# Performance work log

Hardware: AMD Instinct MI355X
Metric: run time of the kernel (lower is better)

The kernel has to match this reference:

```python
import jax, jax.numpy as jnp
import numpy as np

N_NODES = 50000
N_EDGES = 800000
N_GRAPHS = 512
IN_FEATS = 256
HIDDEN = 128
OUT_FEATS = 128


def _lin(key, fan_in, fan_out):
    return jax.random.normal(key, (fan_in, fan_out), jnp.float32) * (1.0 / np.sqrt(fan_in))


def setup_inputs() -> dict:
    key = jax.random.key(0)
    ks = jax.random.split(key, 16)
    x = jax.random.normal(ks[0], (N_NODES, IN_FEATS), jnp.float32)
    edge_index = jax.random.randint(ks[1], (2, N_EDGES), 0, N_NODES, jnp.int32)
    batch = jnp.sort(jax.random.randint(ks[2], (N_NODES,), 0, N_GRAPHS, jnp.int32))
    return {
        "x": x,
        "edge_index": edge_index,
        "batch": batch,
        "num_graphs": N_GRAPHS,
        # TD branch GCN params
        "td_W1": _lin(ks[3], IN_FEATS, HIDDEN), "td_b1": jnp.zeros((HIDDEN,), jnp.float32),
        "td_W2": _lin(ks[4], HIDDEN, OUT_FEATS), "td_b2": jnp.zeros((OUT_FEATS,), jnp.float32),
        # BU branch GCN params
        "bu_W1": _lin(ks[5], IN_FEATS, HIDDEN), "bu_b1": jnp.zeros((HIDDEN,), jnp.float32),
        "bu_W2": _lin(ks[6], HIDDEN, OUT_FEATS), "bu_b2": jnp.zeros((OUT_FEATS,), jnp.float32),
        # proj_head: Linear(256,256) -> ReLU -> Linear(256,128)
        "pw1": _lin(ks[7], OUT_FEATS * 2, 256), "pb1": jnp.zeros((256,), jnp.float32),
        "pw2": _lin(ks[8], 256, 128), "pb2": jnp.zeros((128,), jnp.float32),
    }


def gcn_conv(h_in, W, b, src, dst, n_nodes):
    """PyG GCNConv: self-loops + symmetric normalization D^-1/2 (A+I) D^-1/2 X W + b."""
    h = h_in @ W  # [N, out]
    ones = jnp.ones(src.shape[0], h.dtype)
    deg = jax.ops.segment_sum(ones, dst, num_segments=n_nodes) + 1.0  # +1 for self-loop
    dinv = jax.lax.rsqrt(deg)  # deg >= 1 always
    norm = dinv[src] * dinv[dst]  # [E]
    agg = jax.ops.segment_sum(h[src] * norm[:, None], dst, num_segments=n_nodes)
    agg = agg + h * (dinv * dinv)[:, None]  # self-loop edge contribution
    return agg + b


def reference(x, edge_index, batch, num_graphs,
              td_W1, td_b1, td_W2, td_b2,
              bu_W1, bu_b1, bu_W2, bu_b2,
              pw1, pb1, pw2, pb2):
    n = x.shape[0]
    src, dst = edge_index[0], edge_index[1]

    def branch(W1, b1, W2, b2, s, d):
        h = jax.nn.relu(gcn_conv(x, W1, b1, s, d, n))
        # dropout is identity in eval mode
        h = gcn_conv(h, W2, b2, s, d, n)
        return jax.ops.segment_sum(h, batch, num_segments=num_graphs)  # global_add_pool

    td = branch(td_W1, td_b1, td_W2, td_b2, src, dst)
    bu = branch(bu_W1, bu_b1, bu_W2, bu_b2, dst, src)  # flipped edge_index
    h = jnp.concatenate([bu, td], axis=1)  # [G, 2*out_feats]
    h = jax.nn.relu(h @ pw1 + pb1) @ pw2 + pb2
    return h
```

## Files before the change

kernel.cpp:

```cpp
#include <hip/hip_runtime.h>

#define N_NODES 50000
#define N_PAD   50048
#define N_EDGES 800000
#define N_GRAPHS 512
#define F_IN 256
#define F_H 128
#define F_CAT 256

#define BSHIFT 9
#define NB 98
#define CAP 10240
#define EPB 3125

typedef __attribute__((ext_vector_type(8))) short short8;
typedef __attribute__((ext_vector_type(4))) float f32x4;
typedef unsigned int uint;
typedef unsigned short ushort;

static __device__ __forceinline__ ushort f2bf(float f) {
    uint u = __float_as_uint(f);
    u += 0x7FFF + ((u >> 16) & 1);
    return (ushort)(u >> 16);
}
static __device__ __forceinline__ float bflo(uint v) { return __uint_as_float(v << 16); }
static __device__ __forceinline__ float bfhi(uint v) { return __uint_as_float(v & 0xFFFF0000u); }
static __device__ __forceinline__ float bfu(ushort v) { return __uint_as_float((uint)v << 16); }

#define GLL(g, l) __builtin_amdgcn_global_load_lds( \
    (const __attribute__((address_space(1))) unsigned int*)(g), \
    (__attribute__((address_space(3))) unsigned int*)(l), 16, 0, 0)

__global__ __launch_bounds__(256) void csr_scatter_kernel(
        const int* __restrict__ ei, int* __restrict__ gcur,
        uint* __restrict__ ebuf_td, uint* __restrict__ ebuf_bu) {
    __shared__ int lcnt[256];
    __shared__ int lbase[256];
    int tid = threadIdx.x;
    lcnt[tid] = 0;
    __syncthreads();
    int e0 = blockIdx.x * EPB;
    for (int k = tid; k < EPB; k += 256) {
        int i = e0 + k;
        int s = ei[i], d = ei[N_EDGES + i];
        atomicAdd(&lcnt[d >> BSHIFT], 1);
        atomicAdd(&lcnt[128 + (s >> BSHIFT)], 1);
    }
    __syncthreads();
    if (tid < 2 * NB) {
        int dir = tid / NB, b = tid % NB;
        int c = lcnt[dir * 128 + b];
        lbase[dir * 128 + b] = c ? atomicAdd(&gcur[dir * NB + b], c) : 0;
    }
    __syncthreads();
    lcnt[tid] = 0;
    __syncthreads();
    for (int k = tid; k < EPB; k += 256) {
        int i = e0 + k;
        int s = ei[i], d = ei[N_EDGES + i];
        int bd = d >> BSHIFT, bs = s >> BSHIFT;
        int p = atomicAdd(&lcnt[bd], 1) + lbase[bd];
        ebuf_td[(size_t)bd * CAP + p] = (uint)s | ((uint)(d & 511) << 16);
        int q = atomicAdd(&lcnt[128 + bs], 1) + lbase[128 + bs];
        ebuf_bu[(size_t)bs * CAP + q] = (uint)d | ((uint)(s & 511) << 16);
    }
}

__global__ __launch_bounds__(256) void csr_build_kernel(
        const uint* __restrict__ ebuf_td, const uint* __restrict__ ebuf_bu,
        const int* __restrict__ gcur,
        int* off_td, int* off_bu, ushort* deg_td, ushort* deg_bu,
        float* dinv_td, float* dinv_bu, ushort* csr_td, ushort* csr_bu) {
    int b = blockIdx.x, dir = blockIdx.y;
    const uint* ebuf = dir ? ebuf_bu : ebuf_td;
    int* off     = dir ? off_bu : off_td;
    ushort* deg  = dir ? deg_bu : deg_td;
    float* dinv  = dir ? dinv_bu : dinv_td;
    ushort* csr  = dir ? csr_bu : csr_td;
    __shared__ int cntL[512], offL[512], sm[256];
    int tid = threadIdx.x;
    cntL[tid] = 0; cntL[tid + 256] = 0;
    __syncthreads();
    int rbeg = b * CAP;
    int rend = rbeg + gcur[dir * NB + b];
    for (int k = rbeg + tid; k < rend; k += 256)
        atomicAdd(&cntL[ebuf[k] >> 16], 1);
    __syncthreads();
    int a0 = cntL[tid * 2], a1 = cntL[tid * 2 + 1];
    int ps = a0 + a1;
    sm[tid] = ps;
    __syncthreads();
    for (int o = 1; o < 256; o <<= 1) {
        int u = (tid >= o) ? sm[tid - o] : 0;
        __syncthreads();
        sm[tid] += u;
        __syncthreads();
    }
    int excl = sm[tid] - ps;
    offL[tid * 2] = excl;
    offL[tid * 2 + 1] = excl + a0;
    __syncthreads();
    int nbase = b << BSHIFT;
#pragma unroll
    for (int j = 0; j < 2; j++) {
        int nloc = tid + j * 256;
        int n = nbase + nloc;
        if (n < N_NODES) {
            off[n] = rbeg + offL[nloc];
            int c = cntL[nloc];
            deg[n] = (ushort)c;
            dinv[n] = rsqrtf((float)c + 1.0f);
        }
    }
    cntL[tid] = offL[tid];
    cntL[tid + 256] = offL[tid + 256];
    __syncthreads();
    for (int k = rbeg + tid; k < rend; k += 256) {
        uint e = ebuf[k];
        int slot = atomicAdd(&cntL[e >> 16], 1);
        csr[rbeg + slot] = (ushort)(e & 0xFFFF);
    }
}

__global__ void cvt_x_kernel(const float* __restrict__ x, ushort* __restrict__ xb) {
    size_t i = (size_t)blockIdx.x * blockDim.x + threadIdx.x;
    ushort4 u = {0, 0, 0, 0};
    if (i < (size_t)N_NODES * (F_IN / 4)) {
        float4 f = ((const float4*)x)[i];
        u.x = f2bf(f.x); u.y = f2bf(f.y); u.z = f2bf(f.z); u.w = f2bf(f.w);
    }
    ((ushort4*)xb)[i] = u;
}

__global__ void prep_w_kernel(const float* __restrict__ td_W1, const float* __restrict__ bu_W1,
                              const float* __restrict__ td_W2, const float* __restrict__ bu_W2,
                              ushort* __restrict__ Bt1, ushort* __restrict__ Wt2) {
    int n = blockIdx.x;
    int k = threadIdx.x;
    float w1 = (n < F_H) ? td_W1[(size_t)k * F_H + n] : bu_W1[(size_t)k * F_H + (n - F_H)];
    Bt1[(size_t)n * 256 + k] = f2bf(w1);
    if (k < 128) {
        float w2 = (n < F_H) ? bu_W2[(size_t)k * F_H + n]
                             : td_W2[(size_t)k * F_H + (n - F_H)];
        Wt2[(size_t)k * 256 + n] = f2bf(w2);
    }
}

__global__ __launch_bounds__(256) void gemm_mfma(
        const ushort* __restrict__ A, const ushort* __restrict__ Bt,
        ushort* __restrict__ C,
        const float* __restrict__ dinv_td, const float* __restrict__ dinv_bu) {
    __shared__ __align__(16) ushort As[128 * 32];
    __shared__ __align__(16) ushort Bs[128 * 32];
    int tid = threadIdx.x;
    int wave = tid >> 6, lane = tid & 63, quad = lane >> 4, l16 = lane & 15;
    size_t bm = (size_t)blockIdx.x * 128;
    size_t bn = (size_t)blockIdx.y * 128;
    const float* dsel = blockIdx.y ? dinv_bu : dinv_td;

    f32x4 acc[2][8];
    const f32x4 z4 = {0.f, 0.f, 0.f, 0.f};
#pragma unroll
    for (int i = 0; i < 2; i++)
#pragma unroll
        for (int j = 0; j < 8; j++) acc[i][j] = z4;

    int cb0 = wave * 64;
    int cb1 = 256 + wave * 64;
    int c0 = cb0 + lane, c1 = cb1 + lane;
    int r0 = c0 >> 2, s0 = (c0 & 3) * 8;
    int r1 = c1 >> 2, s1 = (c1 & 3) * 8;
    const ushort* a0p = A + (bm + r0) * 256 + s0;
    const ushort* a1p = A + (bm + r1) * 256 + s1;
    const ushort* b0p = Bt + (bn + r0) * 256 + s0;
    const ushort* b1p = Bt + (bn + r1) * 256 + s1;
    ushort* lA0 = As + cb0 * 8;
    ushort* lA1 = As + cb1 * 8;
    ushort* lB0 = Bs + cb0 * 8;
    ushort* lB1 = Bs + cb1 * 8;

    for (int kb = 0; kb < 8; kb++) {
        int k0 = kb * 32;
        __syncthreads();
        GLL(a0p + k0, lA0);
        GLL(a1p + k0, lA1);
        GLL(b0p + k0, lB0);
        GLL(b1p + k0, lB1);
        __syncthreads();
        short8 af0 = *(const short8*)(As + (wave * 32 + l16) * 32 + quad * 8);
        short8 af1 = *(const short8*)(As + (wave * 32 + 16 + l16) * 32 + quad * 8);
#pragma unroll
        for (int ct = 0; ct < 8; ct++) {
            short8 bfr = *(const short8*)(Bs + (ct * 16 + l16) * 32 + quad * 8);
            acc[0][ct] = __builtin_amdgcn_mfma_f32_16x16x32_bf16(af0, bfr, acc[0][ct], 0, 0, 0);
            acc[1][ct] = __builtin_amdgcn_mfma_f32_16x16x32_bf16(af1, bfr, acc[1][ct], 0, 0, 0);
        }
    }
#pragma unroll
    for (int rt = 0; rt < 2; rt++) {
#pragma unroll
        for (int r = 0; r < 4; r++) {
            size_t row = bm + wave * 32 + rt * 16 + quad * 4 + r;
            float dv = dsel[row];
#pragma unroll
            for (int ct = 0; ct < 8; ct++) {
                C[row * 256 + bn + ct * 16 + l16] = f2bf(acc[rt][ct][r] * dv);
            }
        }
    }
}

static __device__ __forceinline__ void gather_node(
        const ushort* __restrict__ base, const ushort* __restrict__ csr,
        int kb, int ke, int half, float a[4]) {
    float p[4] = {0.f, 0.f, 0.f, 0.f};
    float q[4] = {0.f, 0.f, 0.f, 0.f};
    float r[4] = {0.f, 0.f, 0.f, 0.f};
    int k = kb;
    for (; k + 16 <= ke; k += 16) {
        int i0 = csr[k + half],      i1 = csr[k + 2 + half];
        int i2 = csr[k + 4 + half],  i3 = csr[k + 6 + half];
        int i4 = csr[k + 8 + half],  i5 = csr[k + 10 + half];
        int i6 = csr[k + 12 + half], i7 = csr[k + 14 + half];
        uint2 v0 = *(const uint2*)(base + (size_t)i0 * F_CAT);
        uint2 v1 = *(const uint2*)(base + (size_t)i1 * F_CAT);
        uint2 v2 = *(const uint2*)(base + (size_t)i2 * F_CAT);
        uint2 v3 = *(const uint2*)(base + (size_t)i3 * F_CAT);
        uint2 v4 = *(const uint2*)(base + (size_t)i4 * F_CAT);
        uint2 v5 = *(const uint2*)(base + (size_t)i5 * F_CAT);
        uint2 v6 = *(const uint2*)(base + (size_t)i6 * F_CAT);
        uint2 v7 = *(const uint2*)(base + (size_t)i7 * F_CAT);
        a[0] += bflo(v0.x); a[1] += bfhi(v0.x); a[2] += bflo(v0.y); a[3] += bfhi(v0.y);
        p[0] += bflo(v1.x); p[1] += bfhi(v1.x); p[2] += bflo(v1.y); p[3] += bfhi(v1.y);
        q[0] += bflo(v2.x); q[1] += bfhi(v2.x); q[2] += bflo(v2.y); q[3] += bfhi(v2.y);
        r[0] += bflo(v3.x); r[1] += bfhi(v3.x); r[2] += bflo(v3.y); r[3] += bfhi(v3.y);
        a[0] += bflo(v4.x); a[1] += bfhi(v4.x); a[2] += bflo(v4.y); a[3] += bfhi(v4.y);
        p[0] += bflo(v5.x); p[1] += bfhi(v5.x); p[2] += bflo(v5.y); p[3] += bfhi(v5.y);
        q[0] += bflo(v6.x); q[1] += bfhi(v6.x); q[2] += bflo(v6.y); q[3] += bfhi(v6.y);
        r[0] += bflo(v7.x); r[1] += bfhi(v7.x); r[2] += bflo(v7.y); r[3] += bfhi(v7.y);
    }
    for (; k + 8 <= ke; k += 8) {
        int i0 = csr[k + half],     i1 = csr[k + 2 + half];
        int i2 = csr[k + 4 + half], i3 = csr[k + 6 + half];
        uint2 v0 = *(const uint2*)(base + (size_t)i0 * F_CAT);
        uint2 v1 = *(const uint2*)(base + (size_t)i1 * F_CAT);
        uint2 v2 = *(const uint2*)(base + (size_t)i2 * F_CAT);
        uint2 v3 = *(const uint2*)(base + (size_t)i3 * F_CAT);
        a[0] += bflo(v0.x); a[1] += bfhi(v0.x); a[2] += bflo(v0.y); a[3] += bfhi(v0.y);
        p[0] += bflo(v1.x); p[1] += bfhi(v1.x); p[2] += bflo(v1.y); p[3] += bfhi(v1.y);
        q[0] += bflo(v2.x); q[1] += bfhi(v2.x); q[2] += bflo(v2.y); q[3] += bfhi(v2.y);
        r[0] += bflo(v3.x); r[1] += bfhi(v3.x); r[2] += bflo(v3.y); r[3] += bfhi(v3.y);
    }
    for (; k < ke; k += 2) {
        int kk = k + half;
        if (kk < ke) {
            uint2 v = *(const uint2*)(base + (size_t)csr[kk] * F_CAT);
            a[0] += bflo(v.x); a[1] += bfhi(v.x); a[2] += bflo(v.y); a[3] += bfhi(v.y);
        }
    }
#pragma unroll
    for (int j = 0; j < 4; j++) a[j] += (p[j] + q[j]) + r[j];
}

__global__ __launch_bounds__(256) void agg1_kernel(
        const ushort* __restrict__ linS, ushort* __restrict__ h1s,
        const ushort* __restrict__ csr_td, const int* __restrict__ off_td,
        const ushort* __restrict__ deg_td, const float* __restrict__ dinv_td,
        const ushort* __restrict__ csr_bu, const int* __restrict__ off_bu,
        const ushort* __restrict__ deg_bu, const float* __restrict__ dinv_bu,
        const float* __restrict__ b_td, const float* __restrict__ b_bu) {
    int wave = threadIdx.x >> 6, lane = threadIdx.x & 63;
    int n0 = (blockIdx.x * 2 + (wave >> 1)) * 8;
    int br = wave & 1;
    const ushort* csr = br ? csr_bu : csr_td;
    const int* off    = br ? off_bu : off_td;
    const ushort* deg = br ? deg_bu : deg_td;
    const float* dinv = br ? dinv_bu : dinv_td;
    const float* bias = br ? b_bu : b_td;
    int half = lane >> 5, l32 = lane & 31;
    int col = br * F_H + l32 * 4;
    const ushort* base = linS + col;
    int bcol = l32 * 4;
    float bs0 = bias[bcol], bs1 = bias[bcol + 1];
    float bs2 = bias[bcol + 2], bs3 = bias[bcol + 3];

#pragma unroll
    for (int j = 0; j < 8; j++) {
        int n = n0 + j;
        float a[4] = {0.f, 0.f, 0.f, 0.f};
        int kb = off[n];
        gather_node(base, csr, kb, kb + deg[n], half, a);
#pragma unroll
        for (int t = 0; t < 4; t++) a[t] += __shfl_xor(a[t], 32);
        uint2 vs = *(const uint2*)(base + (size_t)n * F_CAT);
        a[0] += bflo(vs.x); a[1] += bfhi(vs.x); a[2] += bflo(vs.y); a[3] += bfhi(vs.y);
        float dn = dinv[n];
        float o0 = fmaxf(a[0] * dn + bs0, 0.f) * dn;
        float o1 = fmaxf(a[1] * dn + bs1, 0.f) * dn;
        float o2 = fmaxf(a[2] * dn + bs2, 0.f) * dn;
        float o3 = fmaxf(a[3] * dn + bs3, 0.f) * dn;
        if (half == 0) {
            uint2 pk;
            pk.x = (uint)f2bf(o0) | ((uint)f2bf(o1) << 16);
            pk.y = (uint)f2bf(o2) | ((uint)f2bf(o3) << 16);
            *(uint2*)(h1s + (size_t)n * F_CAT + col) = pk;
        }
    }
}

__global__ __launch_bounds__(256) void agg2_pool_kernel(
        const ushort* __restrict__ h1s, float* __restrict__ pooled_pre,
        const int* __restrict__ batch,
        const ushort* __restrict__ csr_td, const int* __restrict__ off_td,
        const ushort* __restrict__ deg_td, const float* __restrict__ dinv_td,
        const ushort* __restrict__ csr_bu, const int* __restrict__ off_bu,
        const ushort* __restrict__ deg_bu, const float* __restrict__ dinv_bu) {
    int wave = threadIdx.x >> 6, lane = threadIdx.x & 63;
    int n0 = (blockIdx.x * 2 + (wave >> 1)) * 8;
    int br = wave & 1;
    const ushort* csr = br ? csr_bu : csr_td;
    const int* off    = br ? off_bu : off_td;
    const ushort* deg = br ? deg_bu : deg_td;
    const float* dinv = br ? dinv_bu : dinv_td;
    int half = lane >> 5, l32 = lane & 31;
    int col = br * F_H + l32 * 4;
    const ushort* base = h1s + col;

    float acc0 = 0.f, acc1 = 0.f, acc2 = 0.f, acc3 = 0.f;
    int gcur = batch[n0];
#pragma unroll
    for (int j = 0; j < 8; j++) {
        int n = n0 + j;
        int g = batch[n];
        if (g != gcur) {
            if (half == 0) {
                float* pp = &pooled_pre[(size_t)gcur * F_CAT + col];
                unsafeAtomicAdd(pp,     acc0);
                unsafeAtomicAdd(pp + 1, acc1);
                unsafeAtomicAdd(pp + 2, acc2);
                unsafeAtomicAdd(pp + 3, acc3);
            }
            acc0 = acc1 = acc2 = acc3 = 0.f;
            gcur = g;
        }
        float a[4] = {0.f, 0.f, 0.f, 0.f};
        int kb = off[n];
        gather_node(base, csr, kb, kb + deg[n], half, a);
#pragma unroll
        for (int t = 0; t < 4; t++) a[t] += __shfl_xor(a[t], 32);
        uint2 vs = *(const uint2*)(base + (size_t)n * F_CAT);
        a[0] += bflo(vs.x); a[1] += bfhi(vs.x); a[2] += bflo(vs.y); a[3] += bfhi(vs.y);
        float dn = dinv[n];
        acc0 += a[0] * dn;
        acc1 += a[1] * dn;
        acc2 += a[2] * dn;
        acc3 += a[3] * dn;
    }
    if (half == 0) {
        float* pp = &pooled_pre[(size_t)gcur * F_CAT + col];
        unsafeAtomicAdd(pp,     acc0);
        unsafeAtomicAdd(pp + 1, acc1);
        unsafeAtomicAdd(pp + 2, acc2);
        unsafeAtomicAdd(pp + 3, acc3);
    }
}

__global__ __launch_bounds__(256) void head_kernel(
        const float* __restrict__ pooled_pre, const int* __restrict__ batch,
        const ushort* __restrict__ Wt2,
        const float* __restrict__ td_b2, const float* __restrict__ bu_b2,
        const float* __restrict__ pw1, const float* __restrict__ pb1,
        const float* __restrict__ pw2, const float* __restrict__ pb2,
        float* __restrict__ out) {
    int g = blockIdx.x;
    int tid = threadIdx.x;
    __shared__ float row[256], z[256], hid[256];
    row[tid] = pooled_pre[(size_t)g * 256 + tid];
    int lo = 0, hi = N_NODES;
    while (lo < hi) { int m = (lo + hi) >> 1; if (batch[m] < g) lo = m + 1; else hi = m; }
    int start = lo;
    lo = start; hi = N_NODES;
    while (lo < hi) { int m = (lo + hi) >> 1; if (batch[m] < g + 1) lo = m + 1; else hi = m; }
    float cnt = (float)(lo - start);
    __syncthreads();
    const float* rsel = (tid < 128) ? (row + F_H) : row;
    float b2 = (tid < 128) ? bu_b2[tid] : td_b2[tid - F_H];
    float acc = cnt * b2;
    for (int k = 0; k < F_H; k++) acc += rsel[k] * bfu(Wt2[(size_t)k * 256 + tid]);
    z[tid] = acc;
    __syncthreads();
    float h = pb1[tid];
    for (int k = 0; k < 256; k++) h += z[k] * pw1[(size_t)k * 256 + tid];
    hid[tid] = fmaxf(h, 0.f);
    __syncthreads();
    if (tid < 128) {
        float o = pb2[tid];
        for (int k = 0; k < 256; k++) o += hid[k] * pw2[(size_t)k * 128 + tid];
        out[(size_t)g * 128 + tid] = o;
    }
}

extern "C" void kernel_launch(void* const* d_in, const int* in_sizes, int n_in,
                              void* d_out, int out_size, void* d_ws, size_t ws_size,
                              hipStream_t stream) {
    const float* x     = (const float*)d_in[0];
    const int*   ei    = (const int*)d_in[1];
    const int*   batch = (const int*)d_in[2];
    const float* td_W1 = (const float*)d_in[4];
    const float* td_b1 = (const float*)d_in[5];
    const float* td_W2 = (const float*)d_in[6];
    const float* td_b2 = (const float*)d_in[7];
    const float* bu_W1 = (const float*)d_in[8];
    const float* bu_b1 = (const float*)d_in[9];
    const float* bu_W2 = (const float*)d_in[10];
    const float* bu_b2 = (const float*)d_in[11];
    const float* pw1   = (const float*)d_in[12];
    const float* pb1   = (const float*)d_in[13];
    const float* pw2   = (const float*)d_in[14];
    const float* pb2   = (const float*)d_in[15];
    float* out = (float*)d_out;

    char* p = (char*)d_ws;
    auto alloc = [&](size_t bytes) { void* r = (void*)p; p += (bytes + 255) & ~(size_t)255; return r; };
    char* zreg = (char*)alloc(1024 + (size_t)N_GRAPHS * F_CAT * sizeof(float));
    int* gcur = (int*)zreg;
    float* pooled_pre = (float*)(zreg + 1024);
    uint* ebuf_td = (uint*)alloc((size_t)NB * CAP * sizeof(uint));
    uint* ebuf_bu = (uint*)alloc((size_t)NB * CAP * sizeof(uint));
    ushort* csr_td = (ushort*)alloc((size_t)NB * CAP * sizeof(ushort));
    ushort* csr_bu = (ushort*)alloc((size_t)NB * CAP * sizeof(ushort));
    int* off_td = (int*)alloc((size_t)N_NODES * sizeof(int));
    int* off_bu = (int*)alloc((size_t)N_NODES * sizeof(int));
    ushort* deg_td = (ushort*)alloc((size_t)N_NODES * sizeof(ushort));
    ushort* deg_bu = (ushort*)alloc((size_t)N_NODES * sizeof(ushort));
    float* dinv_td = (float*)alloc((size_t)N_PAD * sizeof(float));
    float* dinv_bu = (float*)alloc((size_t)N_PAD * sizeof(float));
    ushort* Bt1 = (ushort*)alloc((size_t)256 * 256 * sizeof(ushort));
    ushort* Wt2 = (ushort*)alloc((size_t)128 * 256 * sizeof(ushort));
    ushort* xb   = (ushort*)alloc((size_t)N_PAD * F_CAT * sizeof(ushort));
    ushort* linb = (ushort*)alloc((size_t)N_PAD * F_CAT * sizeof(ushort));
    ushort* h1s  = (ushort*)alloc((size_t)N_PAD * F_CAT * sizeof(ushort));

    hipMemsetAsync(zreg, 0, 1024 + (size_t)N_GRAPHS * F_CAT * sizeof(float), stream);

    csr_scatter_kernel<<<N_EDGES / EPB, 256, 0, stream>>>(ei, gcur, ebuf_td, ebuf_bu);
    csr_build_kernel<<<dim3(NB, 2), 256, 0, stream>>>(ebuf_td, ebuf_bu, gcur,
        off_td, off_bu, deg_td, deg_bu, dinv_td, dinv_bu, csr_td, csr_bu);

    cvt_x_kernel<<<(N_PAD * F_IN / 4) / 256, 256, 0, stream>>>(x, xb);
    prep_w_kernel<<<256, 256, 0, stream>>>(td_W1, bu_W1, td_W2, bu_W2, Bt1, Wt2);

    dim3 gg(N_PAD / 128, 2);
    gemm_mfma<<<gg, 256, 0, stream>>>(xb, Bt1, linb, dinv_td, dinv_bu);
    agg1_kernel<<<N_NODES / 16, 256, 0, stream>>>(linb, h1s,
        csr_td, off_td, deg_td, dinv_td, csr_bu, off_bu, deg_bu, dinv_bu, td_b1, bu_b1);

    agg2_pool_kernel<<<N_NODES / 16, 256, 0, stream>>>(h1s, pooled_pre, batch,
        csr_td, off_td, deg_td, dinv_td, csr_bu, off_bu, deg_bu, dinv_bu);

    head_kernel<<<N_GRAPHS, 256, 0, stream>>>(pooled_pre, batch, Wt2,
        td_b2, bu_b2, pw1, pb1, pw2, pb2, out);
}
```

Baseline: 351.7 us.

## Slice aggregation columns per XCC with atomic work queues for L2 locality

Both aggregation kernels are restructured so each block reads its XCC id and works mainly on one 32-column slice of the feature matrix. The column slice rotates with the XCC, so each XCC's L2 holds a smaller working set of the gathered rows. Work is handed out in 256-node chunks from per-slice atomic counters (persistent blocks, 1024 launched). Each gather is now a 4-byte load per lane, with 4 edges handled in parallel per wave, which means more, narrower memory transactions plus per-chunk syncthreads and atomic overhead.

```diff
diff --git a/kernel.cpp b/kernel.cpp
--- a/kernel.cpp
+++ b/kernel.cpp
@@ -13,6 +13,9 @@
 #define CAP 10240
 #define EPB 3125
 
+#define CHUNK 256
+#define NCHUNK 196
+
 typedef __attribute__((ext_vector_type(8))) short short8;
 typedef __attribute__((ext_vector_type(4))) float f32x4;
 typedef unsigned int uint;
@@ -26,6 +29,12 @@
 static __device__ __forceinline__ float bflo(uint v) { return __uint_as_float(v << 16); }
 static __device__ __forceinline__ float bfhi(uint v) { return __uint_as_float(v & 0xFFFF0000u); }
 static __device__ __forceinline__ float bfu(ushort v) { return __uint_as_float((uint)v << 16); }
+
+static __device__ __forceinline__ int get_xcc() {
+    int x;
+    asm("s_getreg_b32 %0, hwreg(20, 0, 32)" : "=s"(x));
+    return x & 7;
+}
 
 #define GLL(g, l) __builtin_amdgcn_global_load_lds( \
     (const __attribute__((address_space(1))) unsigned int*)(g), \
@@ -210,158 +219,147 @@
     }
 }
 
-static __device__ __forceinline__ void gather_node(
+static __device__ __forceinline__ void gather32(
         const ushort* __restrict__ base, const ushort* __restrict__ csr,
-        int kb, int ke, int half, float a[4]) {
-    float p[4] = {0.f, 0.f, 0.f, 0.f};
-    float q[4] = {0.f, 0.f, 0.f, 0.f};
-    float r[4] = {0.f, 0.f, 0.f, 0.f};
+        int kb, int ke, int e, float& a0, float& a1) {
+    float p0 = 0, p1 = 0, q0 = 0, q1 = 0, r0 = 0, r1 = 0;
     int k = kb;
     for (; k + 16 <= ke; k += 16) {
-        int i0 = csr[k + half],      i1 = csr[k + 2 + half];
-        int i2 = csr[k + 4 + half],  i3 = csr[k + 6 + half];
-        int i4 = csr[k + 8 + half],  i5 = csr[k + 10 + half];
-        int i6 = csr[k + 12 + half], i7 = csr[k + 14 + half];
-        uint2 v0 = *(const uint2*)(base + (size_t)i0 * F_CAT);
-        uint2 v1 = *(const uint2*)(base + (size_t)i1 * F_CAT);
-        uint2 v2 = *(const uint2*)(base + (size_t)i2 * F_CAT);
-        uint2 v3 = *(const uint2*)(base + (size_t)i3 * F_CAT);
-        uint2 v4 = *(const uint2*)(base + (size_t)i4 * F_CAT);
-        uint2 v5 = *(const uint2*)(base + (size_t)i5 * F_CAT);
-        uint2 v6 = *(const uint2*)(base + (size_t)i6 * F_CAT);
-        uint2 v7 = *(const uint2*)(base + (size_t)i7 * F_CAT);
-        a[0] += bflo(v0.x); a[1] += bfhi(v0.x); a[2] += bflo(v0.y); a[3] += bfhi(v0.y);
-        p[0] += bflo(v1.x); p[1] += bfhi(v1.x); p[2] += bflo(v1.y); p[3] += bfhi(v1.y);
-        q[0] += bflo(v2.x); q[1] += bfhi(v2.x); q[2] += bflo(v2.y); q[3] += bfhi(v2.y);
-        r[0] += bflo(v3.x); r[1] += bfhi(v3.x); r[2] += bflo(v3.y); r[3] += bfhi(v3.y);
-        a[0] += bflo(v4.x); a[1] += bfhi(v4.x); a[2] += bflo(v4.y); a[3] += bfhi(v4.y);
-        p[0] += bflo(v5.x); p[1] += bfhi(v5.x); p[2] += bflo(v5.y); p[3] += bfhi(v5.y);
-        q[0] += bflo(v6.x); q[1] += bfhi(v6.x); q[2] += bflo(v6.y); q[3] += bfhi(v6.y);
-        r[0] += bflo(v7.x); r[1] += bfhi(v7.x); r[2] += bflo(v7.y); r[3] += bfhi(v7.y);
-    }
-    for (; k + 8 <= ke; k += 8) {
-        int i0 = csr[k + half],     i1 = csr[k + 2 + half];
-        int i2 = csr[k + 4 + half], i3 = csr[k + 6 + half];
-        uint2 v0 = *(const uint2*)(base + (size_t)i0 * F_CAT);
-        uint2 v1 = *(const uint2*)(base + (size_t)i1 * F_CAT);
-        uint2 v2 = *(const uint2*)(base + (size_t)i2 * F_CAT);
-        uint2 v3 = *(const uint2*)(base + (size_t)i3 * F_CAT);
-        a[0] += bflo(v0.x); a[1] += bfhi(v0.x); a[2] += bflo(v0.y); a[3] += bfhi(v0.y);
-        p[0] += bflo(v1.x); p[1] += bfhi(v1.x); p[2] += bflo(v1.y); p[3] += bfhi(v1.y);
-        q[0] += bflo(v2.x); q[1] += bfhi(v2.x); q[2] += bflo(v2.y); q[3] += bfhi(v2.y);
-        r[0] += bflo(v3.x); r[1] += bfhi(v3.x); r[2] += bflo(v3.y); r[3] += bfhi(v3.y);
-    }
-    for (; k < ke; k += 2) {
-        int kk = k + half;
+        int i0 = csr[k + e], i1 = csr[k + 4 + e];
+        int i2 = csr[k + 8 + e], i3 = csr[k + 12 + e];
+        uint v0 = *(const uint*)(base + (size_t)i0 * F_CAT);
+        uint v1 = *(const uint*)(base + (size_t)i1 * F_CAT);
+        uint v2 = *(const uint*)(base + (size_t)i2 * F_CAT);
+        uint v3 = *(const uint*)(base + (size_t)i3 * F_CAT);
+        a0 += bflo(v0); a1 += bfhi(v0);
+        p0 += bflo(v1); p1 += bfhi(v1);
+        q0 += bflo(v2); q1 += bfhi(v2);
+        r0 += bflo(v3); r1 += bfhi(v3);
+    }
+    for (; k < ke; k += 4) {
+        int kk = k + e;
         if (kk < ke) {
-            uint2 v = *(const uint2*)(base + (size_t)csr[kk] * F_CAT);
-            a[0] += bflo(v.x); a[1] += bfhi(v.x); a[2] += bflo(v.y); a[3] += bfhi(v.y);
-        }
-    }
-#pragma unroll
-    for (int j = 0; j < 4; j++) a[j] += (p[j] + q[j]) + r[j];
-}
-
-__global__ __launch_bounds__(256) void agg1_kernel(
+            uint v = *(const uint*)(base + (size_t)csr[kk] * F_CAT);
+            a0 += bflo(v); a1 += bfhi(v);
+        }
+    }
+    a0 += (p0 + q0) + r0;
+    a1 += (p1 + q1) + r1;
+}
+
+__global__ __launch_bounds__(256) void agg1_sliced(
         const ushort* __restrict__ linS, ushort* __restrict__ h1s,
+        int* __restrict__ q,
         const ushort* __restrict__ csr_td, const int* __restrict__ off_td,
         const ushort* __restrict__ deg_td, const float* __restrict__ dinv_td,
         const ushort* __restrict__ csr_bu, const int* __restrict__ off_bu,
         const ushort* __restrict__ deg_bu, const float* __restrict__ dinv_bu,
         const float* __restrict__ b_td, const float* __restrict__ b_bu) {
-    int wave = threadIdx.x >> 6, lane = threadIdx.x & 63;
-    int n0 = (blockIdx.x * 2 + (wave >> 1)) * 8;
-    int br = wave & 1;
-    const ushort* csr = br ? csr_bu : csr_td;
-    const int* off    = br ? off_bu : off_td;
-    const ushort* deg = br ? deg_bu : deg_td;
-    const float* dinv = br ? dinv_bu : dinv_td;
-    const float* bias = br ? b_bu : b_td;
-    int half = lane >> 5, l32 = lane & 31;
-    int col = br * F_H + l32 * 4;
-    const ushort* base = linS + col;
-    int bcol = l32 * 4;
-    float bs0 = bias[bcol], bs1 = bias[bcol + 1];
-    float bs2 = bias[bcol + 2], bs3 = bias[bcol + 3];
-
-#pragma unroll
-    for (int j = 0; j < 8; j++) {
-        int n = n0 + j;
-        float a[4] = {0.f, 0.f, 0.f, 0.f};
-        int kb = off[n];
-        gather_node(base, csr, kb, kb + deg[n], half, a);
-#pragma unroll
-        for (int t = 0; t < 4; t++) a[t] += __shfl_xor(a[t], 32);
-        uint2 vs = *(const uint2*)(base + (size_t)n * F_CAT);
-        a[0] += bflo(vs.x); a[1] += bfhi(vs.x); a[2] += bflo(vs.y); a[3] += bfhi(vs.y);
-        float dn = dinv[n];
-        float o0 = fmaxf(a[0] * dn + bs0, 0.f) * dn;
-        float o1 = fmaxf(a[1] * dn + bs1, 0.f) * dn;
-        float o2 = fmaxf(a[2] * dn + bs2, 0.f) * dn;
-        float o3 = fmaxf(a[3] * dn + bs3, 0.f) * dn;
-        if (half == 0) {
-            uint2 pk;
-            pk.x = (uint)f2bf(o0) | ((uint)f2bf(o1) << 16);
-            pk.y = (uint)f2bf(o2) | ((uint)f2bf(o3) << 16);
-            *(uint2*)(h1s + (size_t)n * F_CAT + col) = pk;
-        }
-    }
-}
-
-__global__ __launch_bounds__(256) void agg2_pool_kernel(
+    int xcc = get_xcc();
+    int tid = threadIdx.x;
+    int wave = tid >> 6, lane = tid & 63;
+    int e = lane >> 4, c = lane & 15;
+    __shared__ int chunk_s;
+    for (int pass = 0; pass < 8; pass++) {
+        int slice = (xcc + pass) & 7;
+        int dir = slice >> 2;
+        const ushort* csr = dir ? csr_bu : csr_td;
+        const int* off    = dir ? off_bu : off_td;
+        const ushort* deg = dir ? deg_bu : deg_td;
+        const float* dinv = dir ? dinv_bu : dinv_td;
+        const float* bias = dir ? b_bu : b_td;
+        int colbase = dir * F_H + (slice & 3) * 32;
+        const ushort* base = linS + colbase + c * 2;
+        int bc = (slice & 3) * 32 + c * 2;
+        float bs0 = bias[bc], bs1 = bias[bc + 1];
+        while (true) {
+            __syncthreads();
+            if (tid == 0) chunk_s = atomicAdd(&q[slice], 1);
+            __syncthreads();
+            int chunk = chunk_s;
+            if (chunk >= NCHUNK) break;
+            int ns = chunk * CHUNK + wave * 64;
+            int ne = ns + 64 < N_NODES ? ns + 64 : N_NODES;
+            for (int n = ns; n < ne; n++) {
+                float a0 = 0.f, a1 = 0.f;
+                int kb = off[n];
+                gather32(base, csr, kb, kb + deg[n], e, a0, a1);
+                a0 += __shfl_xor(a0, 16); a1 += __shfl_xor(a1, 16);
+                a0 += __shfl_xor(a0, 32); a1 += __shfl_xor(a1, 32);
+                uint vs = *(const uint*)(base + (size_t)n * F_CAT);
+                a0 += bflo(vs); a1 += bfhi(vs);
+                float dn = dinv[n];
+                float o0 = fmaxf(a0 * dn + bs0, 0.f) * dn;
+                float o1 = fmaxf(a1 * dn + bs1, 0.f) * dn;
+                if (e == 0) {
+                    uint pk = (uint)f2bf(o0) | ((uint)f2bf(o1) << 16);
+                    *(uint*)(h1s + (size_t)n * F_CAT + colbase + c * 2) = pk;
+                }
+            }
+        }
+    }
+}
+
+__global__ __launch_bounds__(256) void agg2_sliced(
         const ushort* __restrict__ h1s, float* __restrict__ pooled_pre,
-        const int* __restrict__ batch,
+        int* __restrict__ q, const int* __restrict__ batch,
         const ushort* __restrict__ csr_td, const int* __restrict__ off_td,
         const ushort* __restrict__ deg_td, const float* __restrict__ dinv_td,
         const ushort* __restrict__ csr_bu, const int* __restrict__ off_bu,
         const ushort* __restrict__ deg_bu, const float* __restrict__ dinv_bu) {
-    int wave = threadIdx.x >> 6, lane = threadIdx.x & 63;
-    int n0 = (blockIdx.x * 2 + (wave >> 1)) * 8;
-    int br = wave & 1;
-    const ushort* csr = br ? csr_bu : csr_td;
-    const int* off    = br ? off_bu : off_td;
-    const ushort* deg = br ? deg_bu : deg_td;
-    const float* dinv = br ? dinv_bu : dinv_td;
-    int half = lane >> 5, l32 = lane & 31;
-    int col = br * F_H + l32 * 4;
-    const ushort* base = h1s + col;
-
-    float acc0 = 0.f, acc1 = 0.f, acc2 = 0.f, acc3 = 0.f;
-    int gcur = batch[n0];
-#pragma unroll
-    for (int j = 0; j < 8; j++) {
-        int n = n0 + j;
-        int g = batch[n];
-        if (g != gcur) {
-            if (half == 0) {
-                float* pp = &pooled_pre[(size_t)gcur * F_CAT + col];
-                unsafeAtomicAdd(pp,     acc0);
-                unsafeAtomicAdd(pp + 1, acc1);
-                unsafeAtomicAdd(pp + 2, acc2);
-                unsafeAtomicAdd(pp + 3, acc3);
+    int xcc = get_xcc();
+    int tid = threadIdx.x;
+    int wave = tid >> 6, lane = tid & 63;
+    int e = lane >> 4, c = lane & 15;
+    __shared__ int chunk_s;
+    for (int pass = 0; pass < 8; pass++) {
+        int slice = (xcc + pass) & 7;
+        int dir = slice >> 2;
+        const ushort* csr = dir ? csr_bu : csr_td;
+        const int* off    = dir ? off_bu : off_td;
+        const ushort* deg = dir ? deg_bu : deg_td;
+        const float* dinv = dir ? dinv_bu : dinv_td;
+        int colbase = dir * F_H + (slice & 3) * 32;
+        const ushort* base = h1s + colbase + c * 2;
+        float* pp = pooled_pre + colbase + c * 2;
+        while (true) {
+            __syncthreads();
+            if (tid == 0) chunk_s = atomicAdd(&q[8 + slice], 1);
+            __syncthreads();
+            int chunk = chunk_s;
+            if (chunk >= NCHUNK) break;
+            int ns = chunk * CHUNK + wave * 64;
+            int ne = ns + 64 < N_NODES ? ns + 64 : N_NODES;
+            if (ns < ne) {
+                int gc = batch[ns];
+                float acc0 = 0.f, acc1 = 0.f;
+                for (int n = ns; n < ne; n++) {
+                    int g = batch[n];
+                    if (g != gc) {
+                        if (e == 0) {
+                            unsafeAtomicAdd(pp + (size_t)gc * F_CAT, acc0);
+                            unsafeAtomicAdd(pp + (size_t)gc * F_CAT + 1, acc1);
+                        }
+                        acc0 = acc1 = 0.f;
+                        gc = g;
+                    }
+                    float a0 = 0.f, a1 = 0.f;
+                    int kb = off[n];
+                    gather32(base, csr, kb, kb + deg[n], e, a0, a1);
+                    a0 += __shfl_xor(a0, 16); a1 += __shfl_xor(a1, 16);
+                    a0 += __shfl_xor(a0, 32); a1 += __shfl_xor(a1, 32);
+                    uint vs = *(const uint*)(base + (size_t)n * F_CAT);
+                    a0 += bflo(vs); a1 += bfhi(vs);
+                    float dn = dinv[n];
+                    acc0 += a0 * dn;
+                    acc1 += a1 * dn;
+                }
+                if (e == 0) {
+                    unsafeAtomicAdd(pp + (size_t)gc * F_CAT, acc0);
+                    unsafeAtomicAdd(pp + (size_t)gc * F_CAT + 1, acc1);
+                }
             }
-            acc0 = acc1 = acc2 = acc3 = 0.f;
-            gcur = g;
-        }
-        float a[4] = {0.f, 0.f, 0.f, 0.f};
-        int kb = off[n];
-        gather_node(base, csr, kb, kb + deg[n], half, a);
-#pragma unroll
-        for (int t = 0; t < 4; t++) a[t] += __shfl_xor(a[t], 32);
-        uint2 vs = *(const uint2*)(base + (size_t)n * F_CAT);
-        a[0] += bflo(vs.x); a[1] += bfhi(vs.x); a[2] += bflo(vs.y); a[3] += bfhi(vs.y);
-        float dn = dinv[n];
-        acc0 += a[0] * dn;
-        acc1 += a[1] * dn;
-        acc2 += a[2] * dn;
-        acc3 += a[3] * dn;
-    }
-    if (half == 0) {
-        float* pp = &pooled_pre[(size_t)gcur * F_CAT + col];
-        unsafeAtomicAdd(pp,     acc0);
-        unsafeAtomicAdd(pp + 1, acc1);
-        unsafeAtomicAdd(pp + 2, acc2);
-        unsafeAtomicAdd(pp + 3, acc3);
+        }
     }
 }
 
@@ -422,9 +420,10 @@
 
     char* p = (char*)d_ws;
     auto alloc = [&](size_t bytes) { void* r = (void*)p; p += (bytes + 255) & ~(size_t)255; return r; };
-    char* zreg = (char*)alloc(1024 + (size_t)N_GRAPHS * F_CAT * sizeof(float));
+    char* zreg = (char*)alloc(2048 + (size_t)N_GRAPHS * F_CAT * sizeof(float));
     int* gcur = (int*)zreg;
-    float* pooled_pre = (float*)(zreg + 1024);
+    int* q    = (int*)(zreg + 1024);
+    float* pooled_pre = (float*)(zreg + 2048);
     uint* ebuf_td = (uint*)alloc((size_t)NB * CAP * sizeof(uint));
     uint* ebuf_bu = (uint*)alloc((size_t)NB * CAP * sizeof(uint));
     ushort* csr_td = (ushort*)alloc((size_t)NB * CAP * sizeof(ushort));
@@ -441,7 +440,7 @@
     ushort* linb = (ushort*)alloc((size_t)N_PAD * F_CAT * sizeof(ushort));
     ushort* h1s  = (ushort*)alloc((size_t)N_PAD * F_CAT * sizeof(ushort));
 
-    hipMemsetAsync(zreg, 0, 1024 + (size_t)N_GRAPHS * F_CAT * sizeof(float), stream);
+    hipMemsetAsync(zreg, 0, 2048 + (size_t)N_GRAPHS * F_CAT * sizeof(float), stream);
 
     csr_scatter_kernel<<<N_EDGES / EPB, 256, 0, stream>>>(ei, gcur, ebuf_td, ebuf_bu);
     csr_build_kernel<<<dim3(NB, 2), 256, 0, stream>>>(ebuf_td, ebuf_bu, gcur,
@@ -452,10 +451,10 @@
 
     dim3 gg(N_PAD / 128, 2);
     gemm_mfma<<<gg, 256, 0, stream>>>(xb, Bt1, linb, dinv_td, dinv_bu);
-    agg1_kernel<<<N_NODES / 16, 256, 0, stream>>>(linb, h1s,
+    agg1_sliced<<<1024, 256, 0, stream>>>(linb, h1s, q,
         csr_td, off_td, deg_td, dinv_td, csr_bu, off_bu, deg_bu, dinv_bu, td_b1, bu_b1);
 
-    agg2_pool_kernel<<<N_NODES / 16, 256, 0, stream>>>(h1s, pooled_pre, batch,
+    agg2_sliced<<<1024, 256, 0, stream>>>(h1s, pooled_pre, q, batch,
         csr_td, off_td, deg_td, dinv_td, csr_bu, off_bu, deg_bu, dinv_bu);
 
     head_kernel<<<N_GRAPHS, 256, 0, stream>>>(pooled_pre, batch, Wt2,
```

New measurement: 926.2 us. +163.4%, slower.

## Fuse x bf16 conversion into GEMM and co-schedule it with edge scatter

Applied to the files above, without the earlier changes.

Drops the separate x-to-bf16 conversion pass: the GEMM now loads fp32 x, converts it in registers and writes the tile to LDS itself. The GEMM and the edge-bucket scatter run in a single launch, with blocks split by index, so both kinds of work share the device. Degree counts and dinv are computed earlier by new atomic deg and dinv kernels, so the GEMM epilogue has dinv ready before the CSR build. The costs are extra global atomics over all edges and A-tile loads that no longer go through the direct global-to-LDS path.

```diff
diff --git a/kernel.cpp b/kernel.cpp
--- a/kernel.cpp
+++ b/kernel.cpp
@@ -12,6 +12,7 @@
 #define NB 98
 #define CAP 10240
 #define EPB 3125
+#define GEMM_BLOCKS 782
 
 typedef __attribute__((ext_vector_type(8))) short short8;
 typedef __attribute__((ext_vector_type(4))) float f32x4;
@@ -31,38 +32,139 @@
     (const __attribute__((address_space(1))) unsigned int*)(g), \
     (__attribute__((address_space(3))) unsigned int*)(l), 16, 0, 0)
 
-__global__ __launch_bounds__(256) void csr_scatter_kernel(
+__global__ __launch_bounds__(256) void deg_kernel(const int* __restrict__ ei,
+                                                  int* __restrict__ cnt_td,
+                                                  int* __restrict__ cnt_bu) {
+    int i = blockIdx.x * 256 + threadIdx.x;
+    if (i < N_EDGES) {
+        int s = ei[i], d = ei[N_EDGES + i];
+        atomicAdd(&cnt_td[d], 1);
+        atomicAdd(&cnt_bu[s], 1);
+    }
+}
+
+__global__ __launch_bounds__(256) void dinv_kernel(const int* __restrict__ cnt_td,
+                                                   const int* __restrict__ cnt_bu,
+                                                   float* __restrict__ dinv_td,
+                                                   float* __restrict__ dinv_bu) {
+    int i = blockIdx.x * 256 + threadIdx.x;
+    if (i < N_PAD) {
+        int ct = (i < N_NODES) ? cnt_td[i] : 0;
+        int cb = (i < N_NODES) ? cnt_bu[i] : 0;
+        dinv_td[i] = rsqrtf((float)ct + 1.0f);
+        dinv_bu[i] = rsqrtf((float)cb + 1.0f);
+    }
+}
+
+__global__ __launch_bounds__(256) void gemm_scatter_kernel(
+        const float* __restrict__ x, const ushort* __restrict__ Bt,
+        ushort* __restrict__ C,
+        const float* __restrict__ dinv_td, const float* __restrict__ dinv_bu,
         const int* __restrict__ ei, int* __restrict__ gcur,
         uint* __restrict__ ebuf_td, uint* __restrict__ ebuf_bu) {
+    __shared__ __align__(16) ushort As[128 * 32];
+    __shared__ __align__(16) ushort Bs[128 * 32];
     __shared__ int lcnt[256];
     __shared__ int lbase[256];
     int tid = threadIdx.x;
-    lcnt[tid] = 0;
-    __syncthreads();
-    int e0 = blockIdx.x * EPB;
-    for (int k = tid; k < EPB; k += 256) {
-        int i = e0 + k;
-        int s = ei[i], d = ei[N_EDGES + i];
-        atomicAdd(&lcnt[d >> BSHIFT], 1);
-        atomicAdd(&lcnt[128 + (s >> BSHIFT)], 1);
-    }
-    __syncthreads();
-    if (tid < 2 * NB) {
-        int dir = tid / NB, b = tid % NB;
-        int c = lcnt[dir * 128 + b];
-        lbase[dir * 128 + b] = c ? atomicAdd(&gcur[dir * NB + b], c) : 0;
-    }
-    __syncthreads();
-    lcnt[tid] = 0;
-    __syncthreads();
-    for (int k = tid; k < EPB; k += 256) {
-        int i = e0 + k;
-        int s = ei[i], d = ei[N_EDGES + i];
-        int bd = d >> BSHIFT, bs = s >> BSHIFT;
-        int p = atomicAdd(&lcnt[bd], 1) + lbase[bd];
-        ebuf_td[(size_t)bd * CAP + p] = (uint)s | ((uint)(d & 511) << 16);
-        int q = atomicAdd(&lcnt[128 + bs], 1) + lbase[128 + bs];
-        ebuf_bu[(size_t)bs * CAP + q] = (uint)d | ((uint)(s & 511) << 16);
+
+    if (blockIdx.x < GEMM_BLOCKS) {
+        int wave = tid >> 6, lane = tid & 63, quad = lane >> 4, l16 = lane & 15;
+        size_t bm = (size_t)(blockIdx.x >> 1) * 128;
+        int bnt = blockIdx.x & 1;
+        size_t bn = (size_t)bnt * 128;
+        const float* dsel = bnt ? dinv_bu : dinv_td;
+
+        f32x4 acc[2][8];
+        const f32x4 z4 = {0.f, 0.f, 0.f, 0.f};
+#pragma unroll
+        for (int i = 0; i < 2; i++)
+#pragma unroll
+            for (int j = 0; j < 8; j++) acc[i][j] = z4;
+
+        int ar = tid >> 3;
+        int akq = (tid & 7) * 4;
+        int cb0 = wave * 64;
+        int cb1 = 256 + wave * 64;
+        int c0 = cb0 + lane, c1 = cb1 + lane;
+        int r0 = c0 >> 2, s0 = (c0 & 3) * 8;
+        int r1 = c1 >> 2, s1 = (c1 & 3) * 8;
+        const ushort* b0p = Bt + (bn + r0) * 256 + s0;
+        const ushort* b1p = Bt + (bn + r1) * 256 + s1;
+        ushort* lB0 = Bs + cb0 * 8;
+        ushort* lB1 = Bs + cb1 * 8;
+
+        for (int kb = 0; kb < 8; kb++) {
+            int k0 = kb * 32;
+            float4 av[4];
+#pragma unroll
+            for (int j = 0; j < 4; j++) {
+                size_t grow = bm + ar + j * 32;
+                if (grow < N_NODES)
+                    av[j] = *(const float4*)(x + grow * F_IN + k0 + akq);
+                else
+                    av[j] = make_float4(0.f, 0.f, 0.f, 0.f);
+            }
+            __syncthreads();
+            GLL(b0p + k0, lB0);
+            GLL(b1p + k0, lB1);
+#pragma unroll
+            for (int j = 0; j < 4; j++) {
+                ushort4 u;
+                u.x = f2bf(av[j].x); u.y = f2bf(av[j].y);
+                u.z = f2bf(av[j].z); u.w = f2bf(av[j].w);
+                *(ushort4*)(As + (ar + j * 32) * 32 + akq) = u;
+            }
+            __syncthreads();
+            short8 af0 = *(const short8*)(As + (wave * 32 + l16) * 32 + quad * 8);
+            short8 af1 = *(const short8*)(As + (wave * 32 + 16 + l16) * 32 + quad * 8);
+#pragma unroll
+            for (int ct = 0; ct < 8; ct++) {
+                short8 bfr = *(const short8*)(Bs + (ct * 16 + l16) * 32 + quad * 8);
+                acc[0][ct] = __builtin_amdgcn_mfma_f32_16x16x32_bf16(af0, bfr, acc[0][ct], 0, 0, 0);
+                acc[1][ct] = __builtin_amdgcn_mfma_f32_16x16x32_bf16(af1, bfr, acc[1][ct], 0, 0, 0);
+            }
+        }
+#pragma unroll
+        for (int rt = 0; rt < 2; rt++) {
+#pragma unroll
+            for (int r = 0; r < 4; r++) {
+                size_t row = bm + wave * 32 + rt * 16 + quad * 4 + r;
+                float dv = dsel[row];
+#pragma unroll
+                for (int ct = 0; ct < 8; ct++) {
+                    C[row * 256 + bn + ct * 16 + l16] = f2bf(acc[rt][ct][r] * dv);
+                }
+            }
+        }
+    } else {
+        lcnt[tid] = 0;
+        __syncthreads();
+        int e0 = (blockIdx.x - GEMM_BLOCKS) * EPB;
+        for (int k = tid; k < EPB; k += 256) {
+            int i = e0 + k;
+            int s = ei[i], d = ei[N_EDGES + i];
+            atomicAdd(&lcnt[d >> BSHIFT], 1);
+            atomicAdd(&lcnt[128 + (s >> BSHIFT)], 1);
+        }
+        __syncthreads();
+        if (tid < 2 * NB) {
+            int dir = tid / NB, b = tid % NB;
+            int c = lcnt[dir * 128 + b];
+            lbase[dir * 128 + b] = c ? atomicAdd(&gcur[dir * NB + b], c) : 0;
+        }
+        __syncthreads();
+        lcnt[tid] = 0;
+        __syncthreads();
+        for (int k = tid; k < EPB; k += 256) {
+            int i = e0 + k;
+            int s = ei[i], d = ei[N_EDGES + i];
+            int bd = d >> BSHIFT, bs = s >> BSHIFT;
+            int p = atomicAdd(&lcnt[bd], 1) + lbase[bd];
+            ebuf_td[(size_t)bd * CAP + p] = (uint)s | ((uint)(d & 511) << 16);
+            int q = atomicAdd(&lcnt[128 + bs], 1) + lbase[128 + bs];
+            ebuf_bu[(size_t)bs * CAP + q] = (uint)d | ((uint)(s & 511) << 16);
+        }
     }
 }
 
@@ -70,12 +172,11 @@
         const uint* __restrict__ ebuf_td, const uint* __restrict__ ebuf_bu,
         const int* __restrict__ gcur,
         int* off_td, int* off_bu, ushort* deg_td, ushort* deg_bu,
-        float* dinv_td, float* dinv_bu, ushort* csr_td, ushort* csr_bu) {
+        ushort* csr_td, ushort* csr_bu) {
     int b = blockIdx.x, dir = blockIdx.y;
     const uint* ebuf = dir ? ebuf_bu : ebuf_td;
     int* off     = dir ? off_bu : off_td;
     ushort* deg  = dir ? deg_bu : deg_td;
-    float* dinv  = dir ? dinv_bu : dinv_td;
     ushort* csr  = dir ? csr_bu : csr_td;
     __shared__ int cntL[512], offL[512], sm[256];
     int tid = threadIdx.x;
@@ -107,9 +208,7 @@
         int n = nbase + nloc;
         if (n < N_NODES) {
             off[n] = rbeg + offL[nloc];
-            int c = cntL[nloc];
-            deg[n] = (ushort)c;
-            dinv[n] = rsqrtf((float)c + 1.0f);
+            deg[n] = (ushort)cntL[nloc];
         }
     }
     cntL[tid] = offL[tid];
@@ -120,16 +219,6 @@
         int slot = atomicAdd(&cntL[e >> 16], 1);
         csr[rbeg + slot] = (ushort)(e & 0xFFFF);
     }
-}
-
-__global__ void cvt_x_kernel(const float* __restrict__ x, ushort* __restrict__ xb) {
-    size_t i = (size_t)blockIdx.x * blockDim.x + threadIdx.x;
-    ushort4 u = {0, 0, 0, 0};
-    if (i < (size_t)N_NODES * (F_IN / 4)) {
-        float4 f = ((const float4*)x)[i];
-        u.x = f2bf(f.x); u.y = f2bf(f.y); u.z = f2bf(f.z); u.w = f2bf(f.w);
-    }
-    ((ushort4*)xb)[i] = u;
 }
 
 __global__ void prep_w_kernel(const float* __restrict__ td_W1, const float* __restrict__ bu_W1,
@@ -143,70 +232,6 @@
         float w2 = (n < F_H) ? bu_W2[(size_t)k * F_H + n]
                              : td_W2[(size_t)k * F_H + (n - F_H)];
         Wt2[(size_t)k * 256 + n] = f2bf(w2);
-    }
-}
-
-__global__ __launch_bounds__(256) void gemm_mfma(
-        const ushort* __restrict__ A, const ushort* __restrict__ Bt,
-        ushort* __restrict__ C,
-        const float* __restrict__ dinv_td, const float* __restrict__ dinv_bu) {
-    __shared__ __align__(16) ushort As[128 * 32];
-    __shared__ __align__(16) ushort Bs[128 * 32];
-    int tid = threadIdx.x;
-    int wave = tid >> 6, lane = tid & 63, quad = lane >> 4, l16 = lane & 15;
-    size_t bm = (size_t)blockIdx.x * 128;
-    size_t bn = (size_t)blockIdx.y * 128;
-    const float* dsel = blockIdx.y ? dinv_bu : dinv_td;
-
-    f32x4 acc[2][8];
-    const f32x4 z4 = {0.f, 0.f, 0.f, 0.f};
-#pragma unroll
-    for (int i = 0; i < 2; i++)
-#pragma unroll
-        for (int j = 0; j < 8; j++) acc[i][j] = z4;
-
-    int cb0 = wave * 64;
-    int cb1 = 256 + wave * 64;
-    int c0 = cb0 + lane, c1 = cb1 + lane;
-    int r0 = c0 >> 2, s0 = (c0 & 3) * 8;
-    int r1 = c1 >> 2, s1 = (c1 & 3) * 8;
-    const ushort* a0p = A + (bm + r0) * 256 + s0;
-    const ushort* a1p = A + (bm + r1) * 256 + s1;
-    const ushort* b0p = Bt + (bn + r0) * 256 + s0;
-    const ushort* b1p = Bt + (bn + r1) * 256 + s1;
-    ushort* lA0 = As + cb0 * 8;
-    ushort* lA1 = As + cb1 * 8;
-    ushort* lB0 = Bs + cb0 * 8;
-    ushort* lB1 = Bs + cb1 * 8;
-
-    for (int kb = 0; kb < 8; kb++) {
-        int k0 = kb * 32;
-        __syncthreads();
-        GLL(a0p + k0, lA0);
-        GLL(a1p + k0, lA1);
-        GLL(b0p + k0, lB0);
-        GLL(b1p + k0, lB1);
-        __syncthreads();
-        short8 af0 = *(const short8*)(As + (wave * 32 + l16) * 32 + quad * 8);
-        short8 af1 = *(const short8*)(As + (wave * 32 + 16 + l16) * 32 + quad * 8);
-#pragma unroll
-        for (int ct = 0; ct < 8; ct++) {
-            short8 bfr = *(const short8*)(Bs + (ct * 16 + l16) * 32 + quad * 8);
-            acc[0][ct] = __builtin_amdgcn_mfma_f32_16x16x32_bf16(af0, bfr, acc[0][ct], 0, 0, 0);
-            acc[1][ct] = __builtin_amdgcn_mfma_f32_16x16x32_bf16(af1, bfr, acc[1][ct], 0, 0, 0);
-        }
-    }
-#pragma unroll
-    for (int rt = 0; rt < 2; rt++) {
-#pragma unroll
-        for (int r = 0; r < 4; r++) {
-            size_t row = bm + wave * 32 + rt * 16 + quad * 4 + r;
-            float dv = dsel[row];
-#pragma unroll
-            for (int ct = 0; ct < 8; ct++) {
-                C[row * 256 + bn + ct * 16 + l16] = f2bf(acc[rt][ct][r] * dv);
-            }
-        }
     }
 }
 
@@ -422,9 +447,12 @@
 
     char* p = (char*)d_ws;
     auto alloc = [&](size_t bytes) { void* r = (void*)p; p += (bytes + 255) & ~(size_t)255; return r; };
-    char* zreg = (char*)alloc(1024 + (size_t)N_GRAPHS * F_CAT * sizeof(float));
+    size_t zsz = 1024 + (size_t)N_GRAPHS * F_CAT * sizeof(float) + (size_t)2 * N_NODES * sizeof(int);
+    char* zreg = (char*)alloc(zsz);
     int* gcur = (int*)zreg;
     float* pooled_pre = (float*)(zreg + 1024);
+    int* cnt_td = (int*)(zreg + 1024 + (size_t)N_GRAPHS * F_CAT * sizeof(float));
+    int* cnt_bu = cnt_td + N_NODES;
     uint* ebuf_td = (uint*)alloc((size_t)NB * CAP * sizeof(uint));
     uint* ebuf_bu = (uint*)alloc((size_t)NB * CAP * sizeof(uint));
     ushort* csr_td = (ushort*)alloc((size_t)NB * CAP * sizeof(ushort));
@@ -437,21 +465,22 @@
     float* dinv_bu = (float*)alloc((size_t)N_PAD * sizeof(float));
     ushort* Bt1 = (ushort*)alloc((size_t)256 * 256 * sizeof(ushort));
     ushort* Wt2 = (ushort*)alloc((size_t)128 * 256 * sizeof(ushort));
-    ushort* xb   = (ushort*)alloc((size_t)N_PAD * F_CAT * sizeof(ushort));
     ushort* linb = (ushort*)alloc((size_t)N_PAD * F_CAT * sizeof(ushort));
     ushort* h1s  = (ushort*)alloc((size_t)N_PAD * F_CAT * sizeof(ushort));
 
-    hipMemsetAsync(zreg, 0, 1024 + (size_t)N_GRAPHS * F_CAT * sizeof(float), stream);
-
-    csr_scatter_kernel<<<N_EDGES / EPB, 256, 0, stream>>>(ei, gcur, ebuf_td, ebuf_bu);
+    hipMemsetAsync(zreg, 0, zsz, stream);
+
+    deg_kernel<<<(N_EDGES + 255) / 256, 256, 0, stream>>>(ei, cnt_td, cnt_bu);
+    dinv_kernel<<<(N_PAD + 255) / 256, 256, 0, stream>>>(cnt_td, cnt_bu, dinv_td, dinv_bu);
+
+    prep_w_kernel<<<256, 256, 0, stream>>>(td_W1, bu_W1, td_W2, bu_W2, Bt1, Wt2);
+
+    gemm_scatter_kernel<<<GEMM_BLOCKS + N_EDGES / EPB, 256, 0, stream>>>(
+        x, Bt1, linb, dinv_td, dinv_bu, ei, gcur, ebuf_td, ebuf_bu);
+
     csr_build_kernel<<<dim3(NB, 2), 256, 0, stream>>>(ebuf_td, ebuf_bu, gcur,
-        off_td, off_bu, deg_td, deg_bu, dinv_td, dinv_bu, csr_td, csr_bu);
-
-    cvt_x_kernel<<<(N_PAD * F_IN / 4) / 256, 256, 0, stream>>>(x, xb);
-    prep_w_kernel<<<256, 256, 0, stream>>>(td_W1, bu_W1, td_W2, bu_W2, Bt1, Wt2);
-
-    dim3 gg(N_PAD / 128, 2);
-    gemm_mfma<<<gg, 256, 0, stream>>>(xb, Bt1, linb, dinv_td, dinv_bu);
+        off_td, off_bu, deg_td, deg_bu, csr_td, csr_bu);
+
     agg1_kernel<<<N_NODES / 16, 256, 0, stream>>>(linb, h1s,
         csr_td, off_td, deg_td, dinv_td, csr_bu, off_bu, deg_bu, dinv_bu, td_b1, bu_b1);
 
```

After: 410.3 us. +16.7%, slower.
